# Kernel tuning notes

Hardware: AMD Instinct MI355X
Metric: run time of the kernel (lower is better)

## Reference

```python
import jax, jax.numpy as jnp
import numpy as np

NEG_SLOPE = 0.01  # torch F.leaky_relu default

def _leaky(v):
    return jnp.where(v > 0, v, NEG_SLOPE * v)

def _gcn_conv(h, W, b, row, col, n_nodes):
    # PyG GCNConv with add_self_loops=True, symmetric normalization:
    # out = D^{-1/2} (A + I) D^{-1/2} (h @ W) + b,  deg includes self loop (+1)
    xw = h @ W                                            # [N, H]
    deg = jnp.zeros((n_nodes,), xw.dtype).at[col].add(1.0) + 1.0
    dis = jax.lax.rsqrt(deg)
    norm = dis[row] * dis[col]                            # [E]
    agg = jnp.zeros_like(xw).at[col].add(norm[:, None] * xw[row])
    agg = agg + xw * (1.0 / deg)[:, None]                 # self-loop term: dis_i^2 = 1/deg_i
    return agg + b

def setup_inputs() -> dict:
    key = jax.random.key(0)
    ks = jax.random.split(key, 16)
    N, E, EL = 100000, 1600000, 200000
    IN, H, EA = 256, 64, 8
    s = 0.05
    return {
        "x": jax.random.normal(ks[0], (N, IN), jnp.float32),
        "edge_index": jax.random.randint(ks[1], (2, E), 0, N, jnp.int64),
        "edge_label_index": jax.random.randint(ks[2], (2, EL), 0, N, jnp.int64),
        "edge_attr": jax.random.normal(ks[3], (EL, EA), jnp.float32),
        "W1": jax.random.normal(ks[4], (IN, 128), jnp.float32) * s,
        "b1": jnp.zeros((128,), jnp.float32),
        "W2": jax.random.normal(ks[5], (128, H), jnp.float32) * s,
        "b2": jnp.zeros((H,), jnp.float32),
        "Wg1": jax.random.normal(ks[6], (H, H), jnp.float32) * s,
        "bg1": jnp.zeros((H,), jnp.float32),
        "Wg2": jax.random.normal(ks[7], (H, H), jnp.float32) * s,
        "bg2": jnp.zeros((H,), jnp.float32),
        "Wp": jax.random.normal(ks[8], (2 * H + EA, 1), jnp.float32) * s,
        "bp": jnp.zeros((1,), jnp.float32),
    }

def reference(x, edge_index, edge_label_index, edge_attr,
              W1, b1, W2, b2, Wg1, bg1, Wg2, bg2, Wp, bp):
    n_nodes = x.shape[0]
    row, col = edge_index[0], edge_index[1]
    # preprocess MLP (dropout p=0.0 -> identity)
    h = _leaky(x @ W1 + b1)
    h = _leaky(h @ W2 + b2)
    # two GCN layers
    h = _leaky(_gcn_conv(h, Wg1, bg1, row, col, n_nodes))
    h = _leaky(_gcn_conv(h, Wg2, bg2, row, col, n_nodes))
    # edge scoring head: gather-concat-linear
    h_src = h[edge_label_index[0]]
    h_dst = h[edge_label_index[1]]
    combined = jnp.concatenate([h_src, h_dst, edge_attr], axis=1)
    out = (combined @ Wp + bp).reshape(-1)
    return (out, h)
```

## Files before the change

kernel.cpp:

```cpp
#include <hip/hip_runtime.h>
#include <hip/hip_bf16.h>

typedef __attribute__((ext_vector_type(8))) short bf16x8;
typedef __attribute__((ext_vector_type(4))) float f32x4;

#define BSHIFT 8
#define BW 256
#define NSTR 8
#define BCAP 768
#define LCAP 24
#define KEDGE 16

__device__ __forceinline__ float lk(float v) { return v > 0.f ? v : 0.01f * v; }

__device__ __forceinline__ short f2b(float v) {
  union { __hip_bfloat16 h; short s; } u;
  u.h = __float2bfloat16(v);
  return u.s;
}
__device__ __forceinline__ float loadF(const void* p, size_t i, int f32) {
  return f32 ? ((const float*)p)[i]
             : __bfloat162float(((const __hip_bfloat16*)p)[i]);
}
__device__ __forceinline__ void storeF(void* p, size_t i, int f32, float v) {
  if (f32) ((float*)p)[i] = v;
  else     ((__hip_bfloat16*)p)[i] = __float2bfloat16(v);
}
__device__ __forceinline__ int loadI(const int* p, size_t base, size_t e, int i64) {
  return i64 ? p[2 * (base + e)] : p[base + e];
}
__device__ __forceinline__ float blo(unsigned u) {
  union { unsigned u; float f; } c; c.u = u << 16; return c.f;
}
__device__ __forceinline__ float bhi(unsigned u) {
  union { unsigned u; float f; } c; c.u = u & 0xffff0000u; return c.f;
}

__global__ void detect_kernel(const unsigned short* __restrict__ x,
                              const int* __restrict__ ei, int* __restrict__ flags) {
  int t = threadIdx.x;
  unsigned short u = x[t];
  int ex = (u >> 7) & 0xFF;
  if (ex >= 0xC0) atomicOr(&flags[0], 1);
  if (t < 128 && ei[2 * t + 1] != 0) atomicOr(&flags[1], 1);
}

__global__ __launch_bounds__(64) void pack_w_kernel(const void* __restrict__ W,
                                                    __hip_bfloat16* __restrict__ P,
                                                    int N, const int* __restrict__ flags) {
  int f32 = flags[0] != 0;
  int ks = blockIdx.x, ct = blockIdx.y, KS = gridDim.x;
  int lane = threadIdx.x;
  int g = lane >> 4, m = lane & 15;
  size_t base = ((size_t)(ct * KS + ks) * 64 + (size_t)lane) * 8;
#pragma unroll
  for (int j = 0; j < 8; ++j)
    P[base + j] = __float2bfloat16(
        loadF(W, (size_t)(ks * 32 + g * 8 + j) * N + (size_t)(ct * 16 + m), f32));
}


template <int ROWB, int F32>
__device__ __forceinline__ void stage_tile(const char* __restrict__ Ab, char* tile,
                                           int row0, int M, int w, int lane) {
  constexpr int CPR = ROWB / 16;
  constexpr int PERW = 32 * CPR / 4;
#pragma unroll
  for (int i = 0; i < PERW; i += 64) {
    int p = w * PERW + i + lane;
    int r = p / CPR;
    int pc = p - r * CPR;
    int xv = F32 ? ((r & 3) << 1) : (r & 7);
    int gr = row0 + r; if (gr >= M) gr = M - 1;
    const char* src = Ab + (size_t)gr * ROWB + (size_t)(pc ^ xv) * 16;
    char* dst = tile + (size_t)(w * PERW + i) * 16;
    __builtin_amdgcn_global_load_lds(
        (const __attribute__((address_space(1))) void*)src,
        (__attribute__((address_space(3))) void*)dst, 16, 0, 0);
  }
}

template <int KS, int CT, int F32>
__device__ __forceinline__ void tile_core(const char* tile,
                                          const __hip_bfloat16* __restrict__ bbase,
                                          int m, int g, f32x4 (&accs)[2][CT]) {
  constexpr int ROWB = KS * 32 * (F32 ? 4 : 2);
#pragma unroll
  for (int ks = 0; ks < KS; ++ks) {
    bf16x8 a[2];
#pragma unroll
    for (int t = 0; t < 2; ++t) {
      int r = t * 16 + m;
      if constexpr (F32) {
        int c = ks * 8 + g * 2;
        int xv = (r & 3) << 1;
        float4 q0 = *(const float4*)(tile + (size_t)r * ROWB + (size_t)((c ^ xv) * 16));
        float4 q1 = *(const float4*)(tile + (size_t)r * ROWB + (size_t)(((c + 1) ^ xv) * 16));
        a[t][0] = f2b(q0.x); a[t][1] = f2b(q0.y); a[t][2] = f2b(q0.z); a[t][3] = f2b(q0.w);
        a[t][4] = f2b(q1.x); a[t][5] = f2b(q1.y); a[t][6] = f2b(q1.z); a[t][7] = f2b(q1.w);
      } else {
        int c = ks * 4 + g;
        int xv = r & 7;
        a[t] = *(const bf16x8*)(tile + (size_t)r * ROWB + (size_t)((c ^ xv) * 16));
      }
    }
    const __hip_bfloat16* bb = bbase + (size_t)ks * 64 * 8;
#pragma unroll
    for (int cc = 0; cc < CT; ++cc) {
      bf16x8 b = *(const bf16x8*)(bb + (size_t)cc * KS * 64 * 8);
#pragma unroll
      for (int t = 0; t < 2; ++t)
        accs[t][cc] = __builtin_amdgcn_mfma_f32_16x16x32_bf16(a[t], b, accs[t][cc], 0, 0, 0);
    }
  }
}

template <int KS, int CT, int AMODE>
__global__ __launch_bounds__(256) void gemm_tiled(const void* __restrict__ A,
                                                  const __hip_bfloat16* __restrict__ Bp,
                                                  const void* __restrict__ bias,
                                                  void* __restrict__ Out, int out_bf16,
                                                  __hip_bfloat16* __restrict__ Yout,
                                                  const float* __restrict__ dinv,
                                                  int M, int N, int act,
                                                  const int* __restrict__ flags) {
  constexpr int K = KS * 32;
  constexpr int LDSB = 32 * K * (AMODE ? 4 : 2);
  __shared__ char tile[LDSB];
  int f32 = AMODE ? (flags[0] != 0) : 0;
  int lane = threadIdx.x & 63;
  int w = threadIdx.x >> 6;
  int m = lane & 15, g = lane >> 4;
  int row0 = blockIdx.x * 32;

  const char* Ab = (const char*)A;
  if (f32) stage_tile<K * 4, 1>(Ab, tile, row0, M, w, lane);
  else     stage_tile<K * 2, 0>(Ab, tile, row0, M, w, lane);
  __syncthreads();

  const __hip_bfloat16* bbase = Bp + ((size_t)(w * CT) * KS * 64 + (size_t)lane) * 8;
  f32x4 accs[2][CT];
#pragma unroll
  for (int t = 0; t < 2; ++t)
#pragma unroll
    for (int cc = 0; cc < CT; ++cc) accs[t][cc] = (f32x4){0, 0, 0, 0};

  if (f32) tile_core<KS, CT, 1>(tile, bbase, m, g, accs);
  else     tile_core<KS, CT, 0>(tile, bbase, m, g, accs);

  float bv[CT];
#pragma unroll
  for (int cc = 0; cc < CT; ++cc)
    bv[cc] = bias ? loadF(bias, (size_t)((w * CT + cc) * 16 + m), flags[0] != 0) : 0.f;
#pragma unroll
  for (int t = 0; t < 2; ++t) {
#pragma unroll
    for (int r = 0; r < 4; ++r) {
      int ro = row0 + t * 16 + g * 4 + r;
      if (ro < M) {
        float di = Yout ? dinv[ro] : 0.f;
#pragma unroll
        for (int cc = 0; cc < CT; ++cc) {
          int col = (w * CT + cc) * 16 + m;
          float v = accs[t][cc][r] + bv[cc];
          if (act) v = lk(v);
          if (Out) {
            if (out_bf16) ((__hip_bfloat16*)Out)[(size_t)ro * N + col] = __float2bfloat16(v);
            else          ((float*)Out)[(size_t)ro * N + col] = v;
          }
          if (Yout) Yout[(size_t)ro * N + col] = __float2bfloat16(v * di);
        }
      }
    }
  }
}

__global__ __launch_bounds__(256) void bin_kernel(const int* __restrict__ ei,
                                                  int* __restrict__ cur,
                                                  int2* __restrict__ rec,
                                                  int E, int NB,
                                                  const int* __restrict__ flags) {
  extern __shared__ int lds[];
  int* bcnt = lds;
  int* gbase = lds + NB;
  int2* bins = (int2*)(lds + 2 * NB);
  int i64 = flags[1] == 0;
  int stripe = __builtin_amdgcn_s_getreg(63508) & (NSTR - 1);
  int t = threadIdx.x;
  const int perRound = 256 * KEDGE;
  for (int base = blockIdx.x * perRound; base < E; base += gridDim.x * perRound) {
    for (int b = t; b < NB; b += 256) bcnt[b] = 0;
    __syncthreads();
#pragma unroll 1
    for (int k = 0; k < KEDGE; ++k) {
      int i = base + k * 256 + t;
      if (i < E) {
        int r, c;
        if (i64) {
          r = ((const int2*)ei)[i].x;
          c = ((const int2*)ei)[(size_t)E + i].x;
        } else {
          r = ei[i];
          c = ei[(size_t)E + i];
        }
        int b = c >> BSHIFT;
        int pos = atomicAdd(&bcnt[b], 1);
        if (pos < LCAP) {
          bins[b * LCAP + pos] = make_int2(r, c);
        } else {
          int bs = b * NSTR + stripe;
          int slot = atomicAdd(&cur[bs], 1);
          if (slot < BCAP) rec[(size_t)bs * BCAP + slot] = make_int2(r, c);
        }
      }
    }
    __syncthreads();
    for (int b = t; b < NB; b += 256) {
      int n = min(bcnt[b], LCAP);
      if (n > 0) gbase[b] = atomicAdd(&cur[b * NSTR + stripe], n);
    }
    __syncthreads();
    int lane = t & 63, w = t >> 6;
    for (int b = w; b < NB; b += 4) {
      int n = min(bcnt[b], LCAP);
      if (n == 0) continue;
      int gb = gbase[b];
      size_t sb = (size_t)(b * NSTR + stripe) * BCAP;
      if (lane < n && gb + lane < BCAP)
        rec[sb + gb + lane] = bins[b * LCAP + lane];
    }
    __syncthreads();
  }
}

__global__ __launch_bounds__(512) void bucket_scan(const int* __restrict__ cur,
                                                   int* __restrict__ bbase, int NB) {
  __shared__ int lds[512];
  int t = threadIdx.x;
  int tot = 0;
  if (t < NB)
#pragma unroll
    for (int s = 0; s < NSTR; ++s) tot += min(cur[t * NSTR + s], BCAP);
  lds[t] = tot; __syncthreads();
  for (int o = 1; o < 512; o <<= 1) {
    int a = (t >= o) ? lds[t - o] : 0; __syncthreads();
    lds[t] += a; __syncthreads();
  }
  if (t < NB) bbase[t] = lds[t] - tot;
}

__global__ __launch_bounds__(512) void place_kernel(const int2* __restrict__ rec,
                                                    const int* __restrict__ cur,
                                                    const int* __restrict__ bbase,
                                                    int* __restrict__ rowptr,
                                                    int* __restrict__ csr,
                                                    float* __restrict__ dinv, int Nn) {
  int b = blockIdx.x;
  int lo = b << BSHIFT;
  int t = threadIdx.x;
  __shared__ int cnt[BW];
  __shared__ int sc[BW];
  __shared__ int cursor[BW];
  if (t < BW) cnt[t] = 0;
  __syncthreads();
#pragma unroll 1
  for (int s = 0; s < NSTR; ++s) {
    int n = min(cur[b * NSTR + s], BCAP);
    const int2* rp = rec + (size_t)(b * NSTR + s) * BCAP;
    for (int j = t; j < n; j += 512) atomicAdd(&cnt[rp[j].y - lo], 1);
  }
  __syncthreads();
  int v = 0;
  if (t < BW) { v = cnt[t]; sc[t] = v; }
  __syncthreads();
  for (int o = 1; o < BW; o <<= 1) {
    int a = (t >= o && t < BW) ? sc[t - o] : 0;
    __syncthreads();
    if (t < BW) sc[t] += a;
    __syncthreads();
  }
  if (t < BW) {
    int base = bbase[b];
    int col = lo + t;
    if (col < Nn) {
      rowptr[col] = base + sc[t];
      dinv[col] = rsqrtf((float)v + 1.0f);
    }
    cursor[t] = base + sc[t] - v;
  }
  __syncthreads();
#pragma unroll 1
  for (int s = 0; s < NSTR; ++s) {
    int n = min(cur[b * NSTR + s], BCAP);
    const int2* rp = rec + (size_t)(b * NSTR + s) * BCAP;
    for (int j = t; j < n; j += 512) {
      int2 e = rp[j];
      int pos = atomicAdd(&cursor[e.y - lo], 1);
      csr[pos] = e.x;
    }
  }
}

__global__ __launch_bounds__(256) void gather_kernel(const __hip_bfloat16* __restrict__ y,
                                                     const int* __restrict__ csr,
                                                     const int* __restrict__ rowptr,
                                                     const float* __restrict__ dinv,
                                                     const void* __restrict__ bias,
                                                     void* __restrict__ outp, size_t obase,
                                                     int out_use_flag, int Nn,
                                                     float* __restrict__ ssrc,
                                                     float* __restrict__ sdst,
                                                     const void* __restrict__ Wp,
                                                     const int* __restrict__ flags) {
  int f32 = flags[0] != 0;
  int of32 = out_use_flag ? f32 : 0;
  int lane = threadIdx.x & 63;
  int w = (blockIdx.x * blockDim.x + threadIdx.x) >> 6;
  if (2 * w >= Nn) return;
  int half = lane >> 5;
  int hl = lane & 31;
  int hb = half << 5;
  int node = 2 * w + half;
  int alive = node < Nn;
  int nd = alive ? node : Nn - 1;
  int s = (nd == 0) ? 0 : rowptr[nd - 1];
  int e = rowptr[nd];
  if (!alive) e = s;
  const unsigned* yu = (const unsigned*)y;
  float p0a = 0, p1a = 0, p0b = 0, p1b = 0;
  float p0c = 0, p1c = 0, p0d = 0, p1d = 0;
  for (int base = s; base < e; base += 32) {
    int cnt = e - base; if (cnt > 32) cnt = 32;
    int rl = (base + hl < e) ? csr[base + hl] : 0;
    int j = 0;
    for (; j + 8 <= cnt; j += 8) {
      int r0 = __shfl(rl, hb + j + 0, 64);
      int r1 = __shfl(rl, hb + j + 1, 64);
      int r2 = __shfl(rl, hb + j + 2, 64);
      int r3 = __shfl(rl, hb + j + 3, 64);
      int r4 = __shfl(rl, hb + j + 4, 64);
      int r5 = __shfl(rl, hb + j + 5, 64);
      int r6 = __shfl(rl, hb + j + 6, 64);
      int r7 = __shfl(rl, hb + j + 7, 64);
      unsigned u0 = yu[(unsigned)r0 * 32u + hl];
      unsigned u1 = yu[(unsigned)r1 * 32u + hl];
      unsigned u2 = yu[(unsigned)r2 * 32u + hl];
      unsigned u3 = yu[(unsigned)r3 * 32u + hl];
      unsigned u4 = yu[(unsigned)r4 * 32u + hl];
      unsigned u5 = yu[(unsigned)r5 * 32u + hl];
      unsigned u6 = yu[(unsigned)r6 * 32u + hl];
      unsigned u7 = yu[(unsigned)r7 * 32u + hl];
      p0a += blo(u0); p1a += bhi(u0);
      p0b += blo(u1); p1b += bhi(u1);
      p0c += blo(u2); p1c += bhi(u2);
      p0d += blo(u3); p1d += bhi(u3);
      p0a += blo(u4); p1a += bhi(u4);
      p0b += blo(u5); p1b += bhi(u5);
      p0c += blo(u6); p1c += bhi(u6);
      p0d += blo(u7); p1d += bhi(u7);
    }
    for (; j + 4 <= cnt; j += 4) {
      int r0 = __shfl(rl, hb + j + 0, 64);
      int r1 = __shfl(rl, hb + j + 1, 64);
      int r2 = __shfl(rl, hb + j + 2, 64);
      int r3 = __shfl(rl, hb + j + 3, 64);
      unsigned u0 = yu[(unsigned)r0 * 32u + hl];
      unsigned u1 = yu[(unsigned)r1 * 32u + hl];
      unsigned u2 = yu[(unsigned)r2 * 32u + hl];
      unsigned u3 = yu[(unsigned)r3 * 32u + hl];
      p0a += blo(u0); p1a += bhi(u0);
      p0b += blo(u1); p1b += bhi(u1);
      p0c += blo(u2); p1c += bhi(u2);
      p0d += blo(u3); p1d += bhi(u3);
    }
    for (; j < cnt; ++j) {
      int r0 = __shfl(rl, hb + j, 64);
      unsigned u0 = yu[(unsigned)r0 * 32u + hl];
      p0a += blo(u0); p1a += bhi(u0);
    }
  }
  float acc0 = (p0a + p0b) + (p0c + p0d);
  float acc1 = (p1a + p1b) + (p1c + p1d);
  unsigned un = yu[(unsigned)nd * 32u + hl];
  acc0 += blo(un); acc1 += bhi(un);
  float di = dinv[nd];
  int f = hl * 2;
  float v0 = lk(di * acc0 + loadF(bias, (size_t)f, f32));
  float v1 = lk(di * acc1 + loadF(bias, (size_t)(f + 1), f32));
  if (alive) {
    if (of32) {
      *(float2*)((float*)outp + obase + (size_t)node * 64 + f) = make_float2(v0, v1);
    } else {
      union { unsigned u; unsigned short ss[2]; } pk;
      pk.ss[0] = (unsigned short)f2b(v0);
      pk.ss[1] = (unsigned short)f2b(v1);
      *(unsigned*)((__hip_bfloat16*)outp + obase + (size_t)node * 64 + f) = pk.u;
    }
  }
  if (ssrc) {
    float q1 = v0 * loadF(Wp, (size_t)f, f32) + v1 * loadF(Wp, (size_t)(f + 1), f32);
    float q2 = v0 * loadF(Wp, (size_t)(64 + f), f32) + v1 * loadF(Wp, (size_t)(65 + f), f32);
#pragma unroll
    for (int o = 16; o > 0; o >>= 1) {
      q1 += __shfl_down(q1, o, 64);
      q2 += __shfl_down(q2, o, 64);
    }
    if (hl == 0 && alive) { ssrc[node] = q1; sdst[node] = q2; }
  }
}

__global__ __launch_bounds__(256) void edge_head_kernel(void* __restrict__ dout,
                                                        const int* __restrict__ eli,
                                                        const void* __restrict__ ea,
                                                        const float* __restrict__ ssrc,
                                                        const float* __restrict__ sdst,
                                                        const void* __restrict__ Wp,
                                                        const void* __restrict__ bp,
                                                        int EL, const int* __restrict__ flags) {
  int f32 = flags[0] != 0;
  int i64 = flags[1] == 0;
  int tid = blockIdx.x * blockDim.x + threadIdx.x;
  if (tid >= EL) return;
  int s = loadI(eli, 0, (size_t)tid, i64);
  int d = loadI(eli, (size_t)EL, (size_t)tid, i64);
  float acc = ssrc[s] + sdst[d] + loadF(bp, 0, f32);
  if (f32) {
    const float* eap = (const float*)ea + (size_t)tid * 8;
    float4 u0 = *(const float4*)eap;
    float4 u1 = *(const float4*)(eap + 4);
    acc += u0.x * loadF(Wp, 128, 1) + u0.y * loadF(Wp, 129, 1) +
           u0.z * loadF(Wp, 130, 1) + u0.w * loadF(Wp, 131, 1) +
           u1.x * loadF(Wp, 132, 1) + u1.y * loadF(Wp, 133, 1) +
           u1.z * loadF(Wp, 134, 1) + u1.w * loadF(Wp, 135, 1);
  } else {
    bf16x8 u = *(const bf16x8*)((const __hip_bfloat16*)ea + (size_t)tid * 8);
#pragma unroll
    for (int j = 0; j < 8; ++j) {
      union { short s; __hip_bfloat16 h; } cv; cv.s = u[j];
      acc += __bfloat162float(cv.h) * loadF(Wp, (size_t)(128 + j), 0);
    }
  }
  storeF(dout, (size_t)tid, f32, acc);
}

extern "C" void kernel_launch(void* const* d_in, const int* in_sizes, int n_in,
                              void* d_out, int out_size, void* d_ws, size_t ws_size,
                              hipStream_t stream) {
  const void* x   = d_in[0];
  const int* ei   = (const int*)d_in[1];
  const int* eli  = (const int*)d_in[2];
  const void* ea  = d_in[3];
  const void* W1  = d_in[4];
  const void* b1  = d_in[5];
  const void* W2  = d_in[6];
  const void* b2  = d_in[7];
  const void* Wg1 = d_in[8];
  const void* bg1 = d_in[9];
  const void* Wg2 = d_in[10];
  const void* bg2 = d_in[11];
  const void* Wp  = d_in[12];
  const void* bp  = d_in[13];

  const int Nn = in_sizes[0] / 256;
  const int E  = in_sizes[1] / 2;
  const int EL = in_sizes[2] / 2;
  const int NB = (Nn + BW - 1) >> BSHIFT;

  char* ws = (char*)d_ws;
  size_t off = 0;
  auto take = [&](size_t bytes) -> char* {
    char* p = ws + off;
    off = (off + bytes + 255) & ~(size_t)255;
    return p;
  };
  int*   flags  = (int*)take(256);
  int*   cur    = (int*)take((size_t)NB * NSTR * 4);
  int*   bbase  = (int*)take((size_t)NB * 4);
  int*   rowptr = (int*)take((size_t)Nn * 4);
  float* dinv   = (float*)take((size_t)Nn * 4);
  float* ssrc   = (float*)take((size_t)Nn * 4);
  float* sdst   = (float*)take((size_t)Nn * 4);
  int*   csr    = (int*)take((size_t)E * 4);
  int2*  rec    = (int2*)take((size_t)NB * NSTR * BCAP * 8);
  __hip_bfloat16* pW1 = (__hip_bfloat16*)take(256 * 128 * 2);
  __hip_bfloat16* pW2 = (__hip_bfloat16*)take(128 * 64 * 2);
  __hip_bfloat16* pG1 = (__hip_bfloat16*)take(64 * 64 * 2);
  __hip_bfloat16* pG2 = (__hip_bfloat16*)take(64 * 64 * 2);
  char* regionA = take((size_t)Nn * 128 * 4);
  char* regionB = take((size_t)Nn * 64 * 4);
  __hip_bfloat16* h1 = (__hip_bfloat16*)regionA;
  __hip_bfloat16* y = (__hip_bfloat16*)(regionA + (size_t)Nn * 64 * 4);
  __hip_bfloat16* h2 = (__hip_bfloat16*)regionB;
  __hip_bfloat16* h3 = (__hip_bfloat16*)regionB;

  hipMemsetAsync(flags, 0, 256 + (((size_t)NB * NSTR * 4 + 255) & ~(size_t)255), stream);
  detect_kernel<<<1, 256, 0, stream>>>((const unsigned short*)x, ei, flags);

  dim3 b64(64);
  pack_w_kernel<<<dim3(8, 8), b64, 0, stream>>>(W1, pW1, 128, flags);
  pack_w_kernel<<<dim3(4, 4), b64, 0, stream>>>(W2, pW2, 64, flags);
  pack_w_kernel<<<dim3(2, 4), b64, 0, stream>>>(Wg1, pG1, 64, flags);
  pack_w_kernel<<<dim3(2, 4), b64, 0, stream>>>(Wg2, pG2, 64, flags);

  const int ldsbytes = NB * (8 + LCAP * 8);
  const int nbin = (E + 256 * KEDGE - 1) / (256 * KEDGE);
  bin_kernel<<<nbin, 256, ldsbytes, stream>>>(ei, cur, rec, E, NB, flags);
  bucket_scan<<<1, 512, 0, stream>>>(cur, bbase, NB);
  place_kernel<<<NB, 512, 0, stream>>>(rec, cur, bbase, rowptr, csr, dinv, Nn);

  const int tblocks = (Nn + 31) / 32;
  gemm_tiled<8, 2, 1><<<tblocks, 256, 0, stream>>>(x, pW1, b1, h1, 1, nullptr, nullptr,
                                                   Nn, 128, 1, flags);
  gemm_tiled<4, 1, 0><<<tblocks, 256, 0, stream>>>(h1, pW2, b2, h2, 1, nullptr, nullptr,
                                                   Nn, 64, 1, flags);

  const int gwaves = (Nn + 1) / 2;
  const int gblocks = (gwaves + 3) / 4;
  gemm_tiled<2, 1, 0><<<tblocks, 256, 0, stream>>>(h2, pG1, nullptr, nullptr, 0, y, dinv,
                                                   Nn, 64, 0, flags);
  gather_kernel<<<gblocks, 256, 0, stream>>>(y, csr, rowptr, dinv, bg1,
                                             h3, 0, 0, Nn,
                                             nullptr, nullptr, nullptr, flags);

  gemm_tiled<2, 1, 0><<<tblocks, 256, 0, stream>>>(h3, pG2, nullptr, nullptr, 0, y, dinv,
                                                   Nn, 64, 0, flags);
  gather_kernel<<<gblocks, 256, 0, stream>>>(y, csr, rowptr, dinv, bg2,
                                             d_out, (size_t)EL, 1, Nn,
                                             ssrc, sdst, Wp, flags);

  edge_head_kernel<<<(EL + 255) / 256, 256, 0, stream>>>(d_out, eli, ea, ssrc, sdst,
                                                         Wp, bp, EL, flags);
}
```

Measured before the change: 392.1 us.

## Make GEMM kernels persistent with double-buffered LDS tile prefetch

After: 402.6 us. 1.03x slower.

```diff
diff --git a/kernel.cpp b/kernel.cpp
--- a/kernel.cpp
+++ b/kernel.cpp
@@ -59,119 +59,145 @@
         loadF(W, (size_t)(ks * 32 + g * 8 + j) * N + (size_t)(ct * 16 + m), f32));
 }
 
-
-template <int ROWB, int F32>
-__device__ __forceinline__ void stage_tile(const char* __restrict__ Ab, char* tile,
-                                           int row0, int M, int w, int lane) {
-  constexpr int CPR = ROWB / 16;
-  constexpr int PERW = 32 * CPR / 4;
-#pragma unroll
-  for (int i = 0; i < PERW; i += 64) {
-    int p = w * PERW + i + lane;
-    int r = p / CPR;
-    int pc = p - r * CPR;
-    int xv = F32 ? ((r & 3) << 1) : (r & 7);
-    int gr = row0 + r; if (gr >= M) gr = M - 1;
-    const char* src = Ab + (size_t)gr * ROWB + (size_t)(pc ^ xv) * 16;
-    char* dst = tile + (size_t)(w * PERW + i) * 16;
-    __builtin_amdgcn_global_load_lds(
-        (const __attribute__((address_space(1))) void*)src,
-        (__attribute__((address_space(3))) void*)dst, 16, 0, 0);
-  }
-}
-
-template <int KS, int CT, int F32>
-__device__ __forceinline__ void tile_core(const char* tile,
-                                          const __hip_bfloat16* __restrict__ bbase,
-                                          int m, int g, f32x4 (&accs)[2][CT]) {
-  constexpr int ROWB = KS * 32 * (F32 ? 4 : 2);
-#pragma unroll
-  for (int ks = 0; ks < KS; ++ks) {
-    bf16x8 a[2];
-#pragma unroll
-    for (int t = 0; t < 2; ++t) {
-      int r = t * 16 + m;
-      if constexpr (F32) {
-        int c = ks * 8 + g * 2;
-        int xv = (r & 3) << 1;
-        float4 q0 = *(const float4*)(tile + (size_t)r * ROWB + (size_t)((c ^ xv) * 16));
-        float4 q1 = *(const float4*)(tile + (size_t)r * ROWB + (size_t)(((c + 1) ^ xv) * 16));
-        a[t][0] = f2b(q0.x); a[t][1] = f2b(q0.y); a[t][2] = f2b(q0.z); a[t][3] = f2b(q0.w);
-        a[t][4] = f2b(q1.x); a[t][5] = f2b(q1.y); a[t][6] = f2b(q1.z); a[t][7] = f2b(q1.w);
-      } else {
-        int c = ks * 4 + g;
-        int xv = r & 7;
-        a[t] = *(const bf16x8*)(tile + (size_t)r * ROWB + (size_t)((c ^ xv) * 16));
-      }
-    }
-    const __hip_bfloat16* bb = bbase + (size_t)ks * 64 * 8;
-#pragma unroll
-    for (int cc = 0; cc < CT; ++cc) {
-      bf16x8 b = *(const bf16x8*)(bb + (size_t)cc * KS * 64 * 8);
-#pragma unroll
-      for (int t = 0; t < 2; ++t)
-        accs[t][cc] = __builtin_amdgcn_mfma_f32_16x16x32_bf16(a[t], b, accs[t][cc], 0, 0, 0);
-    }
-  }
-}
-
 template <int KS, int CT, int AMODE>
-__global__ __launch_bounds__(256) void gemm_tiled(const void* __restrict__ A,
-                                                  const __hip_bfloat16* __restrict__ Bp,
-                                                  const void* __restrict__ bias,
-                                                  void* __restrict__ Out, int out_bf16,
-                                                  __hip_bfloat16* __restrict__ Yout,
-                                                  const float* __restrict__ dinv,
-                                                  int M, int N, int act,
-                                                  const int* __restrict__ flags) {
+__global__ __launch_bounds__(256) void gemm_pipe(const void* __restrict__ A,
+                                                 const __hip_bfloat16* __restrict__ Bp,
+                                                 const void* __restrict__ bias,
+                                                 void* __restrict__ Out, int out_bf16,
+                                                 __hip_bfloat16* __restrict__ Yout,
+                                                 const float* __restrict__ dinv,
+                                                 int M, int N, int act,
+                                                 const int* __restrict__ flags) {
   constexpr int K = KS * 32;
-  constexpr int LDSB = 32 * K * (AMODE ? 4 : 2);
-  __shared__ char tile[LDSB];
+  constexpr int CPR = K / 8;
+  constexpr int TILEB = 32 * K * 2;
+  constexpr int PPR = K / 8;
+  constexpr int PP = K / 64;
+  __shared__ char lds[2 * TILEB];
   int f32 = AMODE ? (flags[0] != 0) : 0;
-  int lane = threadIdx.x & 63;
-  int w = threadIdx.x >> 6;
+  int tid = threadIdx.x;
+  int lane = tid & 63;
+  int w = tid >> 6;
   int m = lane & 15, g = lane >> 4;
-  int row0 = blockIdx.x * 32;
-
-  const char* Ab = (const char*)A;
-  if (f32) stage_tile<K * 4, 1>(Ab, tile, row0, M, w, lane);
-  else     stage_tile<K * 2, 0>(Ab, tile, row0, M, w, lane);
-  __syncthreads();
+  int nt = (M + 31) >> 5;
+  if ((int)blockIdx.x >= nt) return;
+
+  float4 sr[2 * PP > 0 ? 2 * PP : 2];
+
+  auto loadregs = [&](int t) {
+    const float* Af = (const float*)A;
+    int row0 = t << 5;
+#pragma unroll
+    for (int j = 0; j < PP; ++j) {
+      int q = j * 256 + tid;
+      int r = q / PPR;
+      int pc = q - r * PPR;
+      int gr = row0 + r; if (gr >= M) gr = M - 1;
+      const float* src = Af + (size_t)gr * K + (size_t)pc * 8;
+      sr[2 * j]     = *(const float4*)src;
+      sr[2 * j + 1] = *(const float4*)(src + 4);
+    }
+  };
+  auto cvtwrite = [&](char* buf) {
+#pragma unroll
+    for (int j = 0; j < PP; ++j) {
+      int q = j * 256 + tid;
+      int r = q / PPR;
+      int pc = q - r * PPR;
+      bf16x8 ov;
+      ov[0] = f2b(sr[2 * j].x);     ov[1] = f2b(sr[2 * j].y);
+      ov[2] = f2b(sr[2 * j].z);     ov[3] = f2b(sr[2 * j].w);
+      ov[4] = f2b(sr[2 * j + 1].x); ov[5] = f2b(sr[2 * j + 1].y);
+      ov[6] = f2b(sr[2 * j + 1].z); ov[7] = f2b(sr[2 * j + 1].w);
+      *(bf16x8*)(buf + (size_t)r * (K * 2) + (size_t)((pc ^ (r & 7)) * 16)) = ov;
+    }
+  };
+  auto gstage = [&](int t, char* buf) {
+    int row0 = t << 5;
+    constexpr int PERW = 32 * CPR / 4;
+#pragma unroll
+    for (int i = 0; i < PERW; i += 64) {
+      int p = w * PERW + i + lane;
+      int r = p / CPR;
+      int pc = p - r * CPR;
+      int gr = row0 + r; if (gr >= M) gr = M - 1;
+      const char* src = (const char*)A + (size_t)gr * (K * 2) +
+                        (size_t)((pc ^ (r & 7)) * 16);
+      char* dst = buf + (size_t)(w * PERW + i) * 16;
+      __builtin_amdgcn_global_load_lds(
+          (const __attribute__((address_space(1))) void*)src,
+          (__attribute__((address_space(3))) void*)dst, 16, 0, 0);
+    }
+  };
 
   const __hip_bfloat16* bbase = Bp + ((size_t)(w * CT) * KS * 64 + (size_t)lane) * 8;
-  f32x4 accs[2][CT];
-#pragma unroll
-  for (int t = 0; t < 2; ++t)
-#pragma unroll
-    for (int cc = 0; cc < CT; ++cc) accs[t][cc] = (f32x4){0, 0, 0, 0};
-
-  if (f32) tile_core<KS, CT, 1>(tile, bbase, m, g, accs);
-  else     tile_core<KS, CT, 0>(tile, bbase, m, g, accs);
-
   float bv[CT];
 #pragma unroll
   for (int cc = 0; cc < CT; ++cc)
     bv[cc] = bias ? loadF(bias, (size_t)((w * CT + cc) * 16 + m), flags[0] != 0) : 0.f;
-#pragma unroll
-  for (int t = 0; t < 2; ++t) {
-#pragma unroll
-    for (int r = 0; r < 4; ++r) {
-      int ro = row0 + t * 16 + g * 4 + r;
-      if (ro < M) {
-        float di = Yout ? dinv[ro] : 0.f;
-#pragma unroll
-        for (int cc = 0; cc < CT; ++cc) {
-          int col = (w * CT + cc) * 16 + m;
-          float v = accs[t][cc][r] + bv[cc];
-          if (act) v = lk(v);
-          if (Out) {
-            if (out_bf16) ((__hip_bfloat16*)Out)[(size_t)ro * N + col] = __float2bfloat16(v);
-            else          ((float*)Out)[(size_t)ro * N + col] = v;
+
+  int t0 = blockIdx.x;
+  if (f32) { loadregs(t0); cvtwrite(lds); }
+  else     { gstage(t0, lds); }
+  __syncthreads();
+
+  int cur = 0;
+  for (int t = t0; t < nt; t += gridDim.x) {
+    int tn = t + gridDim.x;
+    int have = tn < nt;
+    char* bufc = lds + cur * TILEB;
+    char* bufn = lds + (cur ^ 1) * TILEB;
+    if (have) { if (f32) loadregs(tn); else gstage(tn, bufn); }
+
+    f32x4 accs[2][CT];
+#pragma unroll
+    for (int tt = 0; tt < 2; ++tt)
+#pragma unroll
+      for (int cc = 0; cc < CT; ++cc) accs[tt][cc] = (f32x4){0, 0, 0, 0};
+#pragma unroll
+    for (int ks = 0; ks < KS; ++ks) {
+      bf16x8 a[2];
+#pragma unroll
+      for (int tt = 0; tt < 2; ++tt) {
+        int r = tt * 16 + m;
+        int c = ks * 4 + g;
+        a[tt] = *(const bf16x8*)(bufc + (size_t)r * (K * 2) +
+                                 (size_t)((c ^ (r & 7)) * 16));
+      }
+      const __hip_bfloat16* bb = bbase + (size_t)ks * 64 * 8;
+#pragma unroll
+      for (int cc = 0; cc < CT; ++cc) {
+        bf16x8 b = *(const bf16x8*)(bb + (size_t)cc * KS * 64 * 8);
+#pragma unroll
+        for (int tt = 0; tt < 2; ++tt)
+          accs[tt][cc] = __builtin_amdgcn_mfma_f32_16x16x32_bf16(a[tt], b, accs[tt][cc], 0, 0, 0);
+      }
+    }
+    int row0 = t << 5;
+#pragma unroll
+    for (int tt = 0; tt < 2; ++tt) {
+#pragma unroll
+      for (int r = 0; r < 4; ++r) {
+        int ro = row0 + tt * 16 + g * 4 + r;
+        if (ro < M) {
+          float di = Yout ? dinv[ro] : 0.f;
+#pragma unroll
+          for (int cc = 0; cc < CT; ++cc) {
+            int col = (w * CT + cc) * 16 + m;
+            float v = accs[tt][cc][r] + bv[cc];
+            if (act) v = lk(v);
+            if (Out) {
+              if (out_bf16) ((__hip_bfloat16*)Out)[(size_t)ro * N + col] = __float2bfloat16(v);
+              else          ((float*)Out)[(size_t)ro * N + col] = v;
+            }
+            if (Yout) Yout[(size_t)ro * N + col] = __float2bfloat16(v * di);
           }
-          if (Yout) Yout[(size_t)ro * N + col] = __float2bfloat16(v * di);
         }
       }
     }
+    if (have && f32) cvtwrite(bufn);
+    __syncthreads();
+    cur ^= 1;
   }
 }
 
@@ -508,22 +534,23 @@
   bucket_scan<<<1, 512, 0, stream>>>(cur, bbase, NB);
   place_kernel<<<NB, 512, 0, stream>>>(rec, cur, bbase, rowptr, csr, dinv, Nn);
 
-  const int tblocks = (Nn + 31) / 32;
-  gemm_tiled<8, 2, 1><<<tblocks, 256, 0, stream>>>(x, pW1, b1, h1, 1, nullptr, nullptr,
-                                                   Nn, 128, 1, flags);
-  gemm_tiled<4, 1, 0><<<tblocks, 256, 0, stream>>>(h1, pW2, b2, h2, 1, nullptr, nullptr,
-                                                   Nn, 64, 1, flags);
+  const int nt = (Nn + 31) / 32;
+  const int pgrid = nt < 1024 ? nt : 1024;
+  gemm_pipe<8, 2, 1><<<pgrid, 256, 0, stream>>>(x, pW1, b1, h1, 1, nullptr, nullptr,
+                                                Nn, 128, 1, flags);
+  gemm_pipe<4, 1, 0><<<pgrid, 256, 0, stream>>>(h1, pW2, b2, h2, 1, nullptr, nullptr,
+                                                Nn, 64, 1, flags);
 
   const int gwaves = (Nn + 1) / 2;
   const int gblocks = (gwaves + 3) / 4;
-  gemm_tiled<2, 1, 0><<<tblocks, 256, 0, stream>>>(h2, pG1, nullptr, nullptr, 0, y, dinv,
-                                                   Nn, 64, 0, flags);
+  gemm_pipe<2, 1, 0><<<pgrid, 256, 0, stream>>>(h2, pG1, nullptr, nullptr, 0, y, dinv,
+                                                Nn, 64, 0, flags);
   gather_kernel<<<gblocks, 256, 0, stream>>>(y, csr, rowptr, dinv, bg1,
                                              h3, 0, 0, Nn,
                                              nullptr, nullptr, nullptr, flags);
 
-  gemm_tiled<2, 1, 0><<<tblocks, 256, 0, stream>>>(h3, pG2, nullptr, nullptr, 0, y, dinv,
-                                                   Nn, 64, 0, flags);
+  gemm_pipe<2, 1, 0><<<pgrid, 256, 0, stream>>>(h3, pG2, nullptr, nullptr, 0, y, dinv,
+                                                Nn, 64, 0, flags);
   gather_kernel<<<gblocks, 256, 0, stream>>>(y, csr, rowptr, dinv, bg2,
                                              d_out, (size_t)EL, 1, Nn,
                                              ssrc, sdst, Wp, flags);
```
